# Performance work log

Hardware: AMD Instinct MI355X
Metric: run time of the kernel (lower is better)

Reference implementation:

```python
import jax, jax.numpy as jnp
import numpy as np

B, N = 512, 128
NFEAT, NHID, NHEADS, HID = 133, 60, 8, 300
FP_DIM, FP2, TASK = 1489, 512, 1
ALPHA = 0.2
NEG = -9e15


def _lin(k, fi, fo):
    s = 1.0 / np.sqrt(fi)
    return jax.random.uniform(k, (fi, fo), minval=-s, maxval=s, dtype=jnp.float32)


def _vec(k, fi, n):
    s = 1.0 / np.sqrt(fi)
    return jax.random.uniform(k, (n,), minval=-s, maxval=s, dtype=jnp.float32)


def setup_inputs() -> dict:
    key = jax.random.key(0)
    ks = jax.random.split(key, 24)
    x = jax.random.normal(ks[0], (B, N, NFEAT), dtype=jnp.float32)
    adj = jax.random.randint(ks[1], (B, N, N), 0, 2, dtype=jnp.int32)
    adj = jnp.maximum(adj, jnp.eye(N, dtype=jnp.int32)[None])  # ensure valid softmax rows
    fp = jax.random.uniform(ks[2], (B, FP_DIM), dtype=jnp.float32)
    # multi-head GAT params (W has no bias; attention vector a split into src/dst halves)
    sW = 1.0 / np.sqrt(NFEAT)
    W_heads = jax.random.uniform(ks[3], (NHEADS, NFEAT, NHID), minval=-sW, maxval=sW, dtype=jnp.float32)
    sa = 1.0 / np.sqrt(2 * NHID)
    a_src = jax.random.uniform(ks[4], (NHEADS, NHID), minval=-sa, maxval=sa, dtype=jnp.float32)
    a_dst = jax.random.uniform(ks[5], (NHEADS, NHID), minval=-sa, maxval=sa, dtype=jnp.float32)
    W_out = _lin(ks[6], NHEADS * NHID, HID)
    ao_src = _vec(ks[7], 2 * HID, HID)
    ao_dst = _vec(ks[8], 2 * HID, HID)
    fc1_w = _lin(ks[9], FP_DIM, FP2); fc1_b = _vec(ks[10], FP_DIM, FP2)
    fc2_w = _lin(ks[11], FP2, HID); fc2_b = _vec(ks[12], FP2, HID)
    fcg_w = _lin(ks[13], HID, HID); fcg_b = _vec(ks[14], HID, HID)
    fcf_w = _lin(ks[15], HID, HID); fcf_b = _vec(ks[16], HID, HID)
    ffn1_w = _lin(ks[17], 2 * HID, HID); ffn1_b = _vec(ks[18], 2 * HID, HID)
    ffn2_w = _lin(ks[19], HID, TASK); ffn2_b = _vec(ks[20], HID, TASK)
    return {"x": x, "adj": adj, "fp": fp, "W_heads": W_heads, "a_src": a_src,
            "a_dst": a_dst, "W_out": W_out, "ao_src": ao_src, "ao_dst": ao_dst,
            "fc1_w": fc1_w, "fc1_b": fc1_b, "fc2_w": fc2_w, "fc2_b": fc2_b,
            "fcg_w": fcg_w, "fcg_b": fcg_b, "fcf_w": fcf_w, "fcf_b": fcf_b,
            "ffn1_w": ffn1_w, "ffn1_b": ffn1_b, "ffn2_w": ffn2_w, "ffn2_b": ffn2_b}


def reference(x, adj, fp, W_heads, a_src, a_dst, W_out, ao_src, ao_dst,
              fc1_w, fc1_b, fc2_w, fc2_b, fcg_w, fcg_b, fcf_w, fcf_b,
              ffn1_w, ffn1_b, ffn2_w, ffn2_b):
    adjm = adj > 0  # [B,N,N]
    # --- multi-head GAT layer (dropout = identity in eval) ---
    Wh = jnp.einsum('bnf,hfo->bhno', x, W_heads)              # [B,H,N,nhid]
    s = jnp.einsum('bhno,ho->bhn', Wh, a_src)
    d = jnp.einsum('bhno,ho->bhn', Wh, a_dst)
    # e_ij = leakyrelu(a . [Wh_i ; Wh_j]) without materializing [N,N,2F]
    e = jax.nn.leaky_relu(s[:, :, :, None] + d[:, :, None, :], ALPHA)
    e = jnp.where(adjm[:, None], e, NEG)
    att = jax.nn.softmax(e, axis=-1)                          # softmax over neighbors j
    hp = jax.nn.elu(jnp.einsum('bhnm,bhmo->bhno', att, Wh))   # concat=True head output
    h = hp.transpose(0, 2, 1, 3).reshape(B, N, NHEADS * NHID)
    # --- output GAT layer (concat=False) ---
    Wo = h @ W_out                                            # [B,N,HID]
    eo = jax.nn.leaky_relu((Wo @ ao_src)[:, :, None] + (Wo @ ao_dst)[:, None, :], ALPHA)
    eo = jnp.where(adjm, eo, NEG)
    ho = jax.nn.softmax(eo, axis=-1) @ Wo
    ho = jax.nn.log_softmax(jax.nn.elu(ho), axis=-1)          # log_softmax over features (dim=1 in torch)
    gat = ho.mean(axis=1)                                     # sum over atoms / atom_size
    # --- FPN branch ---
    f = jax.nn.relu(fp @ fc1_w + fc1_b)
    f = f @ fc2_w + fc2_b
    # --- fusion (gat_scale = 0.5) ---
    g = jax.nn.relu(gat @ fcg_w + fcg_b)
    f = jax.nn.relu(f @ fcf_w + fcf_b)
    z = jnp.concatenate([g, f], axis=1)                       # [B, 2*HID]
    z = jax.nn.relu(z @ ffn1_w + ffn1_b)
    z = z @ ffn2_w + ffn2_b
    return jax.nn.sigmoid(z)                                  # is_classif, eval mode
```

## Files before the change

kernel.cpp:

```cpp
#include <hip/hip_runtime.h>
#include <hip/hip_bf16.h>
#include <math.h>
#include <stdint.h>

#define LRA 0.2f

typedef __attribute__((ext_vector_type(8))) short bf16x8;
typedef __attribute__((ext_vector_type(8))) unsigned short u16x8;
typedef __attribute__((ext_vector_type(4))) float f32x4;
typedef unsigned long long u64;

__device__ __forceinline__ unsigned short f2bf(float v) {
  union { __hip_bfloat16 b; unsigned short u; } c;
  c.b = __float2bfloat16(v);
  return c.u;
}
__device__ __forceinline__ float bf2f(unsigned short h) {
  union { float f; unsigned int u; } a; a.u = ((unsigned int)h) << 16;
  return a.f;
}
__device__ __forceinline__ float warp_sum(float v){
  #pragma unroll
  for (int s = 32; s; s >>= 1) v += __shfl_xor(v, s);
  return v;
}

__global__ __launch_bounds__(256) void k_mask(const int* __restrict__ adj, u64* __restrict__ mg){
  const int t = threadIdx.x, lane = t & 63, w = t >> 6, b = blockIdx.x;
  const int* adjb = adj + (size_t)b * 128 * 128;
  for (int i = w * 32; i < w * 32 + 32; ++i) {
    u64 b0 = __ballot(adjb[i * 128 + lane] > 0);
    u64 b1 = __ballot(adjb[i * 128 + 64 + lane] > 0);
    if (lane == 0) { mg[((size_t)b * 128 + i) * 2] = b0; mg[((size_t)b * 128 + i) * 2 + 1] = b1; }
  }
}

__global__ __launch_bounds__(64) void k_prep1(
    const float* __restrict__ Whw, unsigned short* __restrict__ BH, unsigned short* __restrict__ BL)
{
  const int kt = blockIdx.x, nt = blockIdx.y, l = threadIdx.x;
  const int n = nt * 16 + (l & 15), k0 = kt * 32 + (l >> 4) * 8;
  const int hd = n / 60, j = n - hd * 60;
  uint4 hv, lv;
  unsigned int* hp = (unsigned int*)&hv;
  unsigned int* lp = (unsigned int*)&lv;
  #pragma unroll
  for (int p = 0; p < 4; ++p) {
    unsigned short hh[2], ll[2];
    #pragma unroll
    for (int e = 0; e < 2; ++e) {
      const int k = k0 + p * 2 + e;
      const float v = (n < 480 && k < 133) ? Whw[((size_t)hd * 133 + k) * 60 + j] : 0.f;
      const unsigned short h = f2bf(v);
      hh[e] = h; ll[e] = f2bf(v - bf2f(h));
    }
    hp[p] = hh[0] | ((unsigned int)hh[1] << 16);
    lp[p] = ll[0] | ((unsigned int)ll[1] << 16);
  }
  const size_t off = (((size_t)(kt * 32 + nt)) * 64 + l) * 8;
  *(uint4*)&BH[off] = hv;
  *(uint4*)&BL[off] = lv;
}

__global__ __launch_bounds__(64) void k_prep2(
    const float* __restrict__ W, unsigned short* __restrict__ BH, unsigned short* __restrict__ BL)
{
  const int kt = blockIdx.x, nt = blockIdx.y, l = threadIdx.x;
  const int n = nt * 16 + (l & 15), k0 = kt * 32 + (l >> 4) * 8;
  uint4 hv, lv;
  unsigned int* hp = (unsigned int*)&hv;
  unsigned int* lp = (unsigned int*)&lv;
  #pragma unroll
  for (int p = 0; p < 4; ++p) {
    unsigned short hh[2], ll[2];
    #pragma unroll
    for (int e = 0; e < 2; ++e) {
      const int k = k0 + p * 2 + e;
      const float v = (n < 300 && k < 480) ? W[(size_t)k * 300 + n] : 0.f;
      const unsigned short h = f2bf(v);
      hh[e] = h; ll[e] = f2bf(v - bf2f(h));
    }
    hp[p] = hh[0] | ((unsigned int)hh[1] << 16);
    lp[p] = ll[0] | ((unsigned int)ll[1] << 16);
  }
  const size_t off = (((size_t)(kt * 20 + nt)) * 64 + l) * 8;
  *(uint4*)&BH[off] = hv;
  *(uint4*)&BL[off] = lv;
}

__global__ __launch_bounds__(512) void k_gemm1(
    const float* __restrict__ x,
    const unsigned short* __restrict__ BH, const unsigned short* __restrict__ BL,
    unsigned int* __restrict__ buf1)
{
  __shared__ unsigned int Apk[32][32];
  const int t = threadIdx.x, lane = t & 63, w = t >> 6, r = lane & 15, g = lane >> 4;
  const int b = blockIdx.x >> 2, p = blockIdx.x & 3;
  const int row0 = p * 32;
  const float* xb = x + (size_t)b * 128 * 133;
  unsigned int* slab = buf1 + (size_t)b * 61440;

  f32x4 acc[2][4];
  #pragma unroll
  for (int mt = 0; mt < 2; ++mt)
    #pragma unroll
    for (int ntl = 0; ntl < 4; ++ntl) acc[mt][ntl] = (f32x4){0.f,0.f,0.f,0.f};

  for (int kt = 0; kt < 5; ++kt) {
    if (t < 256) {
      const int row_l = t >> 3, sl = t & 7;
      const int k0 = kt * 32 + sl * 4;
      uint4 pk;
      unsigned int* pp = (unsigned int*)&pk;
      #pragma unroll
      for (int e = 0; e < 4; ++e) {
        const int k = k0 + e;
        const float v = (k < 133) ? xb[(size_t)(row0 + row_l) * 133 + k] : 0.f;
        const unsigned short h = f2bf(v);
        pp[e] = ((unsigned int)h << 16) | f2bf(v - bf2f(h));
      }
      *(uint4*)&Apk[row_l][((sl ^ (row_l & 7)) << 2)] = pk;
    }
    bf16x8 bh[4], bl[4];
    #pragma unroll
    for (int ntl = 0; ntl < 4; ++ntl) {
      const int nt = w * 4 + ntl;
      const size_t off = (((size_t)(kt * 32 + nt)) * 64 + lane) * 8;
      bh[ntl] = *(const bf16x8*)&BH[off];
      bl[ntl] = *(const bf16x8*)&BL[off];
    }
    __syncthreads();
    #pragma unroll
    for (int mt = 0; mt < 2; ++mt) {
      const int row_l = mt * 16 + r, key = r & 7;
      const uint4 p0 = *(const uint4*)&Apk[row_l][(((2*g)   ^ key) << 2)];
      const uint4 p1 = *(const uint4*)&Apk[row_l][(((2*g+1) ^ key) << 2)];
      const unsigned int pw[8] = {p0.x,p0.y,p0.z,p0.w,p1.x,p1.y,p1.z,p1.w};
      bf16x8 ah, al;
      #pragma unroll
      for (int e = 0; e < 8; ++e) { ah[e] = (short)(pw[e] >> 16); al[e] = (short)(pw[e] & 0xffffu); }
      #pragma unroll
      for (int ntl = 0; ntl < 4; ++ntl) {
        acc[mt][ntl] = __builtin_amdgcn_mfma_f32_16x16x32_bf16(ah, bh[ntl], acc[mt][ntl], 0,0,0);
        acc[mt][ntl] = __builtin_amdgcn_mfma_f32_16x16x32_bf16(al, bh[ntl], acc[mt][ntl], 0,0,0);
        acc[mt][ntl] = __builtin_amdgcn_mfma_f32_16x16x32_bf16(ah, bl[ntl], acc[mt][ntl], 0,0,0);
      }
    }
    __syncthreads();
  }
  #pragma unroll
  for (int mt = 0; mt < 2; ++mt)
    #pragma unroll
    for (int ntl = 0; ntl < 4; ++ntl) {
      const int cc = (w * 4 + ntl) * 16 + r;
      if (cc < 480) {
        const int hd = cc / 60, cl = cc - hd * 60;
        uint4 pv;
        unsigned int* pp = (unsigned int*)&pv;
        #pragma unroll
        for (int q = 0; q < 4; ++q) {
          const float v = acc[mt][ntl][q];
          const unsigned short h = f2bf(v);
          pp[q] = ((unsigned int)h << 16) | f2bf(v - bf2f(h));
        }
        *(uint4*)&slab[(size_t)hd * 7680 + (size_t)cl * 128 + row0 + mt * 16 + (g << 2)] = pv;
      }
    }
}

__global__ __launch_bounds__(64) void k_sd1(
    const unsigned int* __restrict__ buf1, const float* __restrict__ asrc,
    const float* __restrict__ adst, float* __restrict__ s1g, float* __restrict__ d1g)
{
  const int lane = threadIdx.x, sl = blockIdx.x, hd = sl & 7;
  const unsigned int* slab = buf1 + (size_t)sl * 7680;
  float s0 = 0.f, s1v = 0.f, d0 = 0.f, d1v = 0.f;
  #pragma unroll 4
  for (int c = 0; c < 60; ++c) {
    const float ac = asrc[hd * 60 + c], dc = adst[hd * 60 + c];
    const unsigned int p0 = slab[c * 128 + lane];
    const unsigned int p1 = slab[c * 128 + 64 + lane];
    const float v0 = bf2f((unsigned short)(p0 >> 16)) + bf2f((unsigned short)(p0 & 0xffffu));
    const float v1 = bf2f((unsigned short)(p1 >> 16)) + bf2f((unsigned short)(p1 & 0xffffu));
    s0 += v0 * ac; d0 += v0 * dc;
    s1v += v1 * ac; d1v += v1 * dc;
  }
  s1g[(size_t)sl * 128 + lane] = s0;      d1g[(size_t)sl * 128 + lane] = d0;
  s1g[(size_t)sl * 128 + 64 + lane] = s1v; d1g[(size_t)sl * 128 + 64 + lane] = d1v;
}

__global__ __launch_bounds__(128) void k_sd2(
    const unsigned int* __restrict__ buf1, const float* __restrict__ aos,
    const float* __restrict__ aod, float* __restrict__ s2g, float* __restrict__ d2g)
{
  const int j = threadIdx.x, b = blockIdx.x;
  const unsigned int* slab = buf1 + (size_t)b * 61440;
  float s = 0.f, d = 0.f;
  #pragma unroll 4
  for (int c = 0; c < 300; ++c) {
    const float ac = aos[c], dc = aod[c];
    const unsigned int pk = slab[(size_t)c * 128 + j];
    const float v = bf2f((unsigned short)(pk >> 16)) + bf2f((unsigned short)(pk & 0xffffu));
    s += v * ac; d += v * dc;
  }
  s2g[(size_t)b * 128 + j] = s;
  d2g[(size_t)b * 128 + j] = d;
}

__device__ __forceinline__ float make_att_frags(
    const float si, const u64 ma, const u64 mb2, const float* darr,
    const int g, bf16x8* pah, bf16x8* pal)
{
  const unsigned int mby[4] = {
    (unsigned int)(ma  >> (g * 8)) & 0xffu,
    (unsigned int)(ma  >> (32 + g * 8)) & 0xffu,
    (unsigned int)(mb2 >> (g * 8)) & 0xffu,
    (unsigned int)(mb2 >> (32 + g * 8)) & 0xffu };
  float ev[4][8];
  float mx = -3e38f;
  #pragma unroll
  for (int kt = 0; kt < 4; ++kt)
    #pragma unroll
    for (int e = 0; e < 8; ++e) {
      const int j = ((kt & 1) * 32) + ((kt >> 1) * 64) + g * 8 + e;
      float v = si + darr[j];
      v = fmaxf(v, LRA * v);
      const float vv = (mby[((kt & 1) << 1) | (kt >> 1)] & (1u << e)) ? v : -3e38f;
      ev[kt][e] = vv;
      mx = fmaxf(mx, vv);
    }
  mx = fmaxf(mx, __shfl_xor(mx, 16));
  mx = fmaxf(mx, __shfl_xor(mx, 32));
  float sum = 0.f;
  #pragma unroll
  for (int kt = 0; kt < 4; ++kt)
    #pragma unroll
    for (int e = 0; e < 8; ++e) {
      const float p = (ev[kt][e] > -1e37f) ? __expf(ev[kt][e] - mx) : 0.f;
      ev[kt][e] = p;
      sum += p;
    }
  sum += __shfl_xor(sum, 16);
  sum += __shfl_xor(sum, 32);
  #pragma unroll
  for (int kt = 0; kt < 4; ++kt) {
    const int ks = ((kt & 1) << 1) | (kt >> 1);
    union { unsigned int u[4]; bf16x8 v; } hw, lw;
    #pragma unroll
    for (int p2 = 0; p2 < 4; ++p2) {
      const float p0 = ev[ks][2 * p2], p1 = ev[ks][2 * p2 + 1];
      const unsigned short h0 = f2bf(p0), h1 = f2bf(p1);
      hw.u[p2] = h0 | ((unsigned int)h1 << 16);
      lw.u[p2] = f2bf(p0 - bf2f(h0)) | ((unsigned int)f2bf(p1 - bf2f(h1)) << 16);
    }
    pah[kt] = hw.v;
    pal[kt] = lw.v;
  }
  return 1.f / sum;
}

__global__ __launch_bounds__(256) void k_att1(
    unsigned int* __restrict__ buf1, const u64* __restrict__ mg,
    const float* __restrict__ s1g, const float* __restrict__ d1g)
{
  __shared__ unsigned short Th[16][64][8], Tl[16][64][8];
  __shared__ float sarr[128], darr[128];
  __shared__ u64 mAr[128], mBr[128];
  const int t = threadIdx.x, lane = t & 63, w = t >> 6, r = lane & 15, g = lane >> 4;
  const int bid = blockIdx.x;
  const int lb = ((bid & 7) << 9) | (bid >> 3);
  const int b = lb >> 3, hd = lb & 7;
  const size_t sl = (size_t)b * 8 + hd;
  unsigned int* slab = buf1 + sl * 7680;

  if (t < 128) {
    sarr[t] = s1g[sl * 128 + t];
    darr[t] = d1g[sl * 128 + t];
    mAr[t] = mg[((size_t)b * 128 + t) * 2];
    mBr[t] = mg[((size_t)b * 128 + t) * 2 + 1];
  }
  #pragma unroll
  for (int ii = 0; ii < 4; ++ii) {
    const int idx = t + ii * 256;
    const int c = idx & 63, jg = idx >> 6;
    uint4 p0 = {0,0,0,0}, p1 = {0,0,0,0};
    if (c < 60) {
      const uint4* src = (const uint4*)&slab[(size_t)c * 128 + jg * 8];
      p0 = src[0]; p1 = src[1];
    }
    const unsigned int pw[8] = {p0.x,p0.y,p0.z,p0.w,p1.x,p1.y,p1.z,p1.w};
    u16x8 hv, lv;
    #pragma unroll
    for (int e = 0; e < 8; ++e) { hv[e] = (unsigned short)(pw[e] >> 16); lv[e] = (unsigned short)(pw[e] & 0xffffu); }
    const int tile = ((c >> 4) << 2) | (jg >> 2);
    const int li = ((jg & 3) << 4) | (c & 15);
    *(u16x8*)&Th[tile][li][0] = hv;
    *(u16x8*)&Tl[tile][li][0] = lv;
  }
  __syncthreads();
  bf16x8 pah[2][4], pal[2][4];
  float inv2[2];
  #pragma unroll
  for (int mt = 0; mt < 2; ++mt) {
    const int i = w * 32 + mt * 16 + r;
    inv2[mt] = make_att_frags(sarr[i], mAr[i], mBr[i], darr, g, pah[mt], pal[mt]);
  }
  f32x4 acc[2][4];
  #pragma unroll
  for (int mt = 0; mt < 2; ++mt)
    #pragma unroll
    for (int nt = 0; nt < 4; ++nt) acc[mt][nt] = (f32x4){0.f,0.f,0.f,0.f};
  #pragma unroll
  for (int kt = 0; kt < 4; ++kt)
    #pragma unroll
    for (int nt = 0; nt < 4; ++nt) {
      const bf16x8 bh = *(const bf16x8*)&Th[(nt << 2) | kt][lane][0];
      const bf16x8 bl = *(const bf16x8*)&Tl[(nt << 2) | kt][lane][0];
      #pragma unroll
      for (int mt = 0; mt < 2; ++mt) {
        acc[mt][nt] = __builtin_amdgcn_mfma_f32_16x16x32_bf16(pah[mt][kt], bh, acc[mt][nt], 0,0,0);
        acc[mt][nt] = __builtin_amdgcn_mfma_f32_16x16x32_bf16(pal[mt][kt], bh, acc[mt][nt], 0,0,0);
        acc[mt][nt] = __builtin_amdgcn_mfma_f32_16x16x32_bf16(pah[mt][kt], bl, acc[mt][nt], 0,0,0);
      }
    }
  #pragma unroll
  for (int mt = 0; mt < 2; ++mt) {
    float sc[4];
    #pragma unroll
    for (int q = 0; q < 4; ++q) sc[q] = __shfl(inv2[mt], g * 4 + q);
    #pragma unroll
    for (int nt = 0; nt < 4; ++nt) {
      const int cc = nt * 16 + r;
      if (cc < 60) {
        #pragma unroll
        for (int q = 0; q < 4; ++q) {
          const int row = w * 32 + mt * 16 + g * 4 + q;
          float v = acc[mt][nt][q] * sc[q];
          v = v > 0.f ? v : __expf(v) - 1.f;
          const unsigned short h = f2bf(v), l = f2bf(v - bf2f(h));
          slab[(size_t)row * 60 + cc] = ((unsigned int)h << 16) | l;
        }
      }
    }
  }
}

__global__ __launch_bounds__(256, 3) void k_gemm2(
    unsigned int* __restrict__ buf1,
    const unsigned short* __restrict__ BH, const unsigned short* __restrict__ BL)
{
  __shared__ unsigned int Apk[64][32];
  const int t = threadIdx.x, lane = t & 63, w = t >> 6, r = lane & 15, g = lane >> 4;
  const int b = blockIdx.x >> 1, p = blockIdx.x & 1;
  const int row0 = p * 64;
  unsigned int* slab = buf1 + (size_t)b * 61440;

  f32x4 acc[4][5];
  #pragma unroll
  for (int mt = 0; mt < 4; ++mt)
    #pragma unroll
    for (int ntl = 0; ntl < 5; ++ntl) acc[mt][ntl] = (f32x4){0.f,0.f,0.f,0.f};

  for (int kt = 0; kt < 15; ++kt) {
    #pragma unroll
    for (int i = 0; i < 2; ++i) {
      const int idx = t + i * 256, row_l = idx >> 3, sl = idx & 7;
      const int k0 = kt * 32 + sl * 4;
      const int hd = k0 / 60, c = k0 - hd * 60;
      const uint4 v = *(const uint4*)&slab[(size_t)hd * 7680 + (size_t)(row0 + row_l) * 60 + c];
      *(uint4*)&Apk[row_l][((sl ^ (row_l & 7)) << 2)] = v;
    }
    bf16x8 bh[5], bl[5];
    #pragma unroll
    for (int ntl = 0; ntl < 5; ++ntl) {
      const int nt = w * 5 + ntl;
      const size_t off = (((size_t)(kt * 20 + nt)) * 64 + lane) * 8;
      bh[ntl] = *(const bf16x8*)&BH[off];
      bl[ntl] = *(const bf16x8*)&BL[off];
    }
    __syncthreads();
    #pragma unroll
    for (int mt = 0; mt < 4; ++mt) {
      const int row_l = mt * 16 + r, key = r & 7;
      const uint4 p0 = *(const uint4*)&Apk[row_l][(((2*g)   ^ key) << 2)];
      const uint4 p1 = *(const uint4*)&Apk[row_l][(((2*g+1) ^ key) << 2)];
      const unsigned int pw[8] = {p0.x,p0.y,p0.z,p0.w,p1.x,p1.y,p1.z,p1.w};
      bf16x8 ah, al;
      #pragma unroll
      for (int e = 0; e < 8; ++e) { ah[e] = (short)(pw[e] >> 16); al[e] = (short)(pw[e] & 0xffffu); }
      #pragma unroll
      for (int ntl = 0; ntl < 5; ++ntl) {
        acc[mt][ntl] = __builtin_amdgcn_mfma_f32_16x16x32_bf16(ah, bh[ntl], acc[mt][ntl], 0,0,0);
        acc[mt][ntl] = __builtin_amdgcn_mfma_f32_16x16x32_bf16(al, bh[ntl], acc[mt][ntl], 0,0,0);
        acc[mt][ntl] = __builtin_amdgcn_mfma_f32_16x16x32_bf16(ah, bl[ntl], acc[mt][ntl], 0,0,0);
      }
    }
    __syncthreads();
  }
  #pragma unroll
  for (int mt = 0; mt < 4; ++mt)
    #pragma unroll
    for (int ntl = 0; ntl < 5; ++ntl) {
      const int cc = w * 80 + ntl * 16 + r;
      if (cc < 300) {
        uint4 pv;
        unsigned int* pp = (unsigned int*)&pv;
        #pragma unroll
        for (int q = 0; q < 4; ++q) {
          const float v = acc[mt][ntl][q];
          const unsigned short h = f2bf(v);
          pp[q] = ((unsigned int)h << 16) | f2bf(v - bf2f(h));
        }
        *(uint4*)&slab[(size_t)cc * 128 + row0 + mt * 16 + (g << 2)] = pv;
      }
    }
}

__global__ __launch_bounds__(256) void k_att2(
    const unsigned int* __restrict__ buf1, const u64* __restrict__ mg,
    const float* __restrict__ s2g, const float* __restrict__ d2g,
    float* __restrict__ gat)
{
  __shared__ unsigned short Th[16][64][8], Tl[16][64][8];
  __shared__ float sarr[128], darr[128];
  __shared__ u64 mAr[128], mBr[128];
  __shared__ float colsum[304];
  __shared__ float srow[16];
  const int t = threadIdx.x, lane = t & 63, w = t >> 6, r = lane & 15, g = lane >> 4;
  const int b = blockIdx.x;
  const unsigned int* slab = buf1 + (size_t)b * 61440;

  if (t < 128) {
    sarr[t] = s2g[(size_t)b * 128 + t];
    darr[t] = d2g[(size_t)b * 128 + t];
    mAr[t] = mg[((size_t)b * 128 + t) * 2];
    mBr[t] = mg[((size_t)b * 128 + t) * 2 + 1];
  }
  for (int c = t; c < 304; c += 256) colsum[c] = 0.f;
  __syncthreads();
  bf16x8 pah[2][4], pal[2][4];
  float inv2[2];
  #pragma unroll
  for (int mt = 0; mt < 2; ++mt) {
    const int i = w * 32 + mt * 16 + r;
    inv2[mt] = make_att_frags(sarr[i], mAr[i], mBr[i], darr, g, pah[mt], pal[mt]);
  }
  float scq[2][4];
  #pragma unroll
  for (int mt = 0; mt < 2; ++mt)
    #pragma unroll
    for (int q = 0; q < 4; ++q) scq[mt][q] = __shfl(inv2[mt], g * 4 + q);

  float m8[2][4], l8[2][4];
  #pragma unroll
  for (int mt = 0; mt < 2; ++mt)
    #pragma unroll
    for (int q = 0; q < 4; ++q) { m8[mt][q] = -3e38f; l8[mt][q] = 0.f; }

  for (int ch = 0; ch < 5; ++ch) {
    #pragma unroll
    for (int ii = 0; ii < 4; ++ii) {
      const int idx = t + ii * 256;
      const int c = idx & 63, jg = idx >> 6;
      const int gc = ch * 64 + c;
      uint4 p0 = {0,0,0,0}, p1 = {0,0,0,0};
      if (gc < 300) {
        const uint4* src = (const uint4*)&slab[(size_t)gc * 128 + jg * 8];
        p0 = src[0]; p1 = src[1];
      }
      const unsigned int pw[8] = {p0.x,p0.y,p0.z,p0.w,p1.x,p1.y,p1.z,p1.w};
      u16x8 hv, lv;
      #pragma unroll
      for (int e = 0; e < 8; ++e) { hv[e] = (unsigned short)(pw[e] >> 16); lv[e] = (unsigned short)(pw[e] & 0xffffu); }
      const int tile = ((c >> 4) << 2) | (jg >> 2);
      const int li = ((jg & 3) << 4) | (c & 15);
      *(u16x8*)&Th[tile][li][0] = hv;
      *(u16x8*)&Tl[tile][li][0] = lv;
    }
    __syncthreads();
    f32x4 pacc[2][4];
    #pragma unroll
    for (int mt = 0; mt < 2; ++mt)
      #pragma unroll
      for (int nt = 0; nt < 4; ++nt) pacc[mt][nt] = (f32x4){0.f,0.f,0.f,0.f};
    #pragma unroll
    for (int kt = 0; kt < 4; ++kt)
      #pragma unroll
      for (int nt = 0; nt < 4; ++nt) {
        const bf16x8 bh = *(const bf16x8*)&Th[(nt << 2) | kt][lane][0];
        const bf16x8 bl = *(const bf16x8*)&Tl[(nt << 2) | kt][lane][0];
        #pragma unroll
        for (int mt = 0; mt < 2; ++mt) {
          pacc[mt][nt] = __builtin_amdgcn_mfma_f32_16x16x32_bf16(pah[mt][kt], bh, pacc[mt][nt], 0,0,0);
          pacc[mt][nt] = __builtin_amdgcn_mfma_f32_16x16x32_bf16(pal[mt][kt], bh, pacc[mt][nt], 0,0,0);
          pacc[mt][nt] = __builtin_amdgcn_mfma_f32_16x16x32_bf16(pah[mt][kt], bl, pacc[mt][nt], 0,0,0);
        }
      }
    float csA[4] = {0,0,0,0};
    #pragma unroll
    for (int mt = 0; mt < 2; ++mt) {
      float vq[4][4];
      #pragma unroll
      for (int nt = 0; nt < 4; ++nt) {
        const int cc = ch * 64 + nt * 16 + r;
        const bool cv = cc < 300;
        #pragma unroll
        for (int q = 0; q < 4; ++q) {
          float v = pacc[mt][nt][q] * scq[mt][q];
          v = v > 0.f ? v : __expf(v) - 1.f;
          vq[nt][q] = cv ? v : -3e38f;
          csA[nt] += cv ? v : 0.f;
        }
      }
      #pragma unroll
      for (int q = 0; q < 4; ++q) {
        float mx = fmaxf(fmaxf(vq[0][q], vq[1][q]), fmaxf(vq[2][q], vq[3][q]));
        mx = fmaxf(mx, __shfl_xor(mx, 1));
        mx = fmaxf(mx, __shfl_xor(mx, 2));
        mx = fmaxf(mx, __shfl_xor(mx, 4));
        mx = fmaxf(mx, __shfl_xor(mx, 8));
        const float nm = fmaxf(m8[mt][q], mx);
        float ps = __expf(vq[0][q]-nm) + __expf(vq[1][q]-nm) + __expf(vq[2][q]-nm) + __expf(vq[3][q]-nm);
        ps += __shfl_xor(ps, 1); ps += __shfl_xor(ps, 2);
        ps += __shfl_xor(ps, 4); ps += __shfl_xor(ps, 8);
        l8[mt][q] = l8[mt][q] * __expf(m8[mt][q] - nm) + ps;
        m8[mt][q] = nm;
      }
    }
    #pragma unroll
    for (int nt = 0; nt < 4; ++nt) {
      float cs = csA[nt];
      cs += __shfl_xor(cs, 16); cs += __shfl_xor(cs, 32);
      const int cc = ch * 64 + nt * 16 + r;
      if (g == 0 && cc < 300) atomicAdd(&colsum[cc], cs);
    }
    __syncthreads();
  }
  if (r == 0) {
    float sp = 0.f;
    #pragma unroll
    for (int mt = 0; mt < 2; ++mt)
      #pragma unroll
      for (int q = 0; q < 4; ++q) sp += m8[mt][q] + __logf(l8[mt][q]);
    srow[w * 4 + g] = sp;
  }
  __syncthreads();
  float S = 0.f;
  #pragma unroll
  for (int k = 0; k < 16; ++k) S += srow[k];
  for (int c = t; c < 300; c += 256)
    gat[(size_t)b * 300 + c] = (colsum[c] - S) * (1.f / 128.f);
}

__global__ __launch_bounds__(256) void k_gemm_sk(
    const float* __restrict__ A, const float* __restrict__ B,
    float* __restrict__ P, int M, int K, int N, int kpt)
{
  __shared__ unsigned short Ah[64][40], Al[64][40], Bh[64][40], Bl[64][40];
  const int t = threadIdx.x, lane = t & 63, w = t >> 6, r = lane & 15, g = lane >> 4;
  const int row0 = blockIdx.x * 64, col0 = blockIdx.y * 64;
  const int sk = blockIdx.z;
  const int k0 = sk * kpt * 32;
  const int kend = min(K, k0 + kpt * 32);

  f32x4 acc[4];
  #pragma unroll
  for (int nt = 0; nt < 4; ++nt) acc[nt] = (f32x4){0.f,0.f,0.f,0.f};

  for (int kt = k0; kt < kend; kt += 32) {
    #pragma unroll
    for (int ii = 0; ii < 2; ++ii) {
      const int idx = t + ii * 256, ar = idx >> 3, aq = (idx & 7) * 4, gk = kt + aq;
      const float* ap = &A[(size_t)(row0 + ar) * K + gk];
      float v0 = gk     < kend ? ap[0] : 0.f;
      float v1 = gk + 1 < kend ? ap[1] : 0.f;
      float v2 = gk + 2 < kend ? ap[2] : 0.f;
      float v3 = gk + 3 < kend ? ap[3] : 0.f;
      unsigned short h0=f2bf(v0),h1=f2bf(v1),h2=f2bf(v2),h3=f2bf(v3);
      *(unsigned int*)&Ah[ar][aq]   = h0 | ((unsigned int)h1 << 16);
      *(unsigned int*)&Ah[ar][aq+2] = h2 | ((unsigned int)h3 << 16);
      unsigned short l0=f2bf(v0-bf2f(h0)),l1=f2bf(v1-bf2f(h1)),l2=f2bf(v2-bf2f(h2)),l3=f2bf(v3-bf2f(h3));
      *(unsigned int*)&Al[ar][aq]   = l0 | ((unsigned int)l1 << 16);
      *(unsigned int*)&Al[ar][aq+2] = l2 | ((unsigned int)l3 << 16);
    }
    #pragma unroll
    for (int ii = 0; ii < 4; ++ii) {
      const int idx = t + ii * 256, n = idx & 63, kk = (idx >> 6) * 2;
      const int gn = col0 + n;
      float v0 = (gn < N && kt + kk     < kend) ? B[(size_t)(kt + kk) * N + gn] : 0.f;
      float v1 = (gn < N && kt + kk + 1 < kend) ? B[(size_t)(kt + kk + 1) * N + gn] : 0.f;
      unsigned short h0 = f2bf(v0), h1 = f2bf(v1);
      *(unsigned int*)&Bh[n][kk] = h0 | ((unsigned int)h1 << 16);
      unsigned short l0 = f2bf(v0 - bf2f(h0)), l1 = f2bf(v1 - bf2f(h1));
      *(unsigned int*)&Bl[n][kk] = l0 | ((unsigned int)l1 << 16);
    }
    __syncthreads();
    const bf16x8 ah  = *(const bf16x8*)&Ah[w * 16 + r][g * 8];
    const bf16x8 al2 = *(const bf16x8*)&Al[w * 16 + r][g * 8];
    #pragma unroll
    for (int nt = 0; nt < 4; ++nt) {
      const bf16x8 bh = *(const bf16x8*)&Bh[nt * 16 + r][g * 8];
      const bf16x8 bl = *(const bf16x8*)&Bl[nt * 16 + r][g * 8];
      acc[nt] = __builtin_amdgcn_mfma_f32_16x16x32_bf16(ah,  bh, acc[nt], 0,0,0);
      acc[nt] = __builtin_amdgcn_mfma_f32_16x16x32_bf16(al2, bh, acc[nt], 0,0,0);
      acc[nt] = __builtin_amdgcn_mfma_f32_16x16x32_bf16(ah,  bl, acc[nt], 0,0,0);
    }
    __syncthreads();
  }
  float* Pout = P + (size_t)sk * M * N;
  #pragma unroll
  for (int nt = 0; nt < 4; ++nt) {
    const int cc = col0 + nt * 16 + r;
    if (cc < N) {
      #pragma unroll
      for (int q = 0; q < 4; ++q)
        Pout[(size_t)(row0 + w * 16 + g * 4 + q) * N + cc] = acc[nt][q];
    }
  }
}

__global__ __launch_bounds__(256) void k_reduce(
    const float* __restrict__ P, const float* __restrict__ bias,
    float* __restrict__ C, int M, int N, int ldc, int nsk, int act)
{
  const int idx = blockIdx.x * 256 + threadIdx.x;
  if (idx >= M * N) return;
  const int row = idx / N, col = idx - row * N;
  float s = bias[col];
  for (int k = 0; k < nsk; ++k) s += P[(size_t)k * M * N + idx];
  if (act) s = fmaxf(s, 0.f);
  C[(size_t)row * ldc + col] = s;
}

__global__ __launch_bounds__(512) void k_out(
    const float* __restrict__ z1, const float* __restrict__ w2,
    const float* __restrict__ b2, float* __restrict__ out)
{
  const int t = threadIdx.x, lane = t & 63, w = t >> 6;
  const int b = blockIdx.x * 8 + w;
  float p = 0.f;
  for (int k = lane; k < 300; k += 64) p += z1[(size_t)b * 300 + k] * w2[k];
  p = warp_sum(p);
  if (lane == 0) out[b] = 1.f / (1.f + __expf(-(p + b2[0])));
}

extern "C" void kernel_launch(void* const* d_in, const int* in_sizes, int n_in,
                              void* d_out, int out_size, void* d_ws, size_t ws_size,
                              hipStream_t stream)
{
  const float* x    = (const float*)d_in[0];
  const int*   adj  = (const int*)d_in[1];
  const float* fp   = (const float*)d_in[2];
  const float* Whw  = (const float*)d_in[3];
  const float* asrc = (const float*)d_in[4];
  const float* adst = (const float*)d_in[5];
  const float* Wout = (const float*)d_in[6];
  const float* aos  = (const float*)d_in[7];
  const float* aod  = (const float*)d_in[8];
  const float* fc1w = (const float*)d_in[9];
  const float* fc1b = (const float*)d_in[10];
  const float* fc2w = (const float*)d_in[11];
  const float* fc2b = (const float*)d_in[12];
  const float* fcgw = (const float*)d_in[13];
  const float* fcgb = (const float*)d_in[14];
  const float* fcfw = (const float*)d_in[15];
  const float* fcfb = (const float*)d_in[16];
  const float* f1w  = (const float*)d_in[17];
  const float* f1b  = (const float*)d_in[18];
  const float* f2w  = (const float*)d_in[19];
  const float* f2b  = (const float*)d_in[20];
  float* out = (float*)d_out;

  char* wsb = (char*)d_ws;
  unsigned int* buf1 = (unsigned int*)wsb;
  float* s1g = (float*)(wsb + 125829120);
  float* d1g = (float*)(wsb + 127926272);
  float* s2g = (float*)(wsb + 130023424);
  float* d2g = (float*)(wsb + 130285568);
  u64*   mgb = (u64*)  (wsb + 130547712);
  float* gatp = (float*)(wsb + 131596288);
  float* fpnp = (float*)(wsb + 132210688);
  float* f1buf = (float*)(wsb + 132825088);
  float* zb    = (float*)(wsb + 133873664);
  float* z1b   = (float*)(wsb + 135102464);
  float* P0 = (float*)(wsb + 135716864);
  float* P1 = (float*)(wsb + 142008320);
  float* P2 = (float*)(wsb + 144465920);
  float* P3 = (float*)(wsb + 145694720);
  float* P4 = (float*)(wsb + 146923520);
  unsigned short* Bf1H = (unsigned short*)(wsb + 149381120);
  unsigned short* Bf1L = (unsigned short*)(wsb + 149544960);
  unsigned short* Bf2H = (unsigned short*)(wsb + 149708800);
  unsigned short* Bf2L = (unsigned short*)(wsb + 150016000);

  k_prep1<<<dim3(5, 32), 64, 0, stream>>>(Whw, Bf1H, Bf1L);
  k_prep2<<<dim3(15, 20), 64, 0, stream>>>(Wout, Bf2H, Bf2L);
  k_mask <<<512, 256, 0, stream>>>(adj, mgb);
  k_gemm1<<<2048, 512, 0, stream>>>(x, Bf1H, Bf1L, buf1);
  k_sd1  <<<4096, 64, 0, stream>>>(buf1, asrc, adst, s1g, d1g);
  k_att1 <<<4096, 256, 0, stream>>>(buf1, mgb, s1g, d1g);
  k_gemm2<<<1024, 256, 0, stream>>>(buf1, Bf2H, Bf2L);
  k_sd2  <<<512, 128, 0, stream>>>(buf1, aos, aod, s2g, d2g);
  k_att2 <<<512, 256, 0, stream>>>(buf1, mgb, s2g, d2g, gatp);
  k_gemm_sk<<<dim3(8,8,6), 256, 0, stream>>>(fp, fc1w, P0, 512, 1489, 512, 8);
  k_reduce<<<1024, 256, 0, stream>>>(P0, fc1b, f1buf, 512, 512, 512, 6, 1);
  k_gemm_sk<<<dim3(8,5,4), 256, 0, stream>>>(f1buf, fc2w, P1, 512, 512, 300, 4);
  k_reduce<<<600, 256, 0, stream>>>(P1, fc2b, fpnp, 512, 300, 300, 4, 0);
  k_gemm_sk<<<dim3(8,5,2), 256, 0, stream>>>(gatp, fcgw, P2, 512, 300, 300, 5);
  k_gemm_sk<<<dim3(8,5,2), 256, 0, stream>>>(fpnp, fcfw, P3, 512, 300, 300, 5);
  k_reduce<<<600, 256, 0, stream>>>(P2, fcgb, zb, 512, 300, 600, 2, 1);
  k_reduce<<<600, 256, 0, stream>>>(P3, fcfb, zb + 300, 512, 300, 600, 2, 1);
  k_gemm_sk<<<dim3(8,5,4), 256, 0, stream>>>(zb, f1w, P4, 512, 600, 300, 5);
  k_reduce<<<600, 256, 0, stream>>>(P4, f1b, z1b, 512, 300, 300, 4, 1);
  k_out<<<64, 512, 0, stream>>>(z1b, f2w, f2b, out);
}
```

Before: 383.8 us.

## Fuse first-layer GEMM, attention scores and per-head attention into one kernel

Replaces the separate k_gemm1, k_sd1 and k_att1 kernels with a single k_fga1 kernel. Each block computes one head's Wh for one graph in registers, derives the src/dst scores from the accumulators with shuffles, and stages the split-bf16 Wh in LDS for the attention MFMA. The intermediate global round-trip of Wh and the score buffers is removed. In exchange, x is reloaded and reconverted eight times (once per head), and the LDS footprint per block is larger.

After: 385.9 us. No clear change (+0.5%).

```diff
diff --git a/kernel.cpp b/kernel.cpp
--- a/kernel.cpp
+++ b/kernel.cpp
@@ -40,7 +40,7 @@
 {
   const int kt = blockIdx.x, nt = blockIdx.y, l = threadIdx.x;
   const int n = nt * 16 + (l & 15), k0 = kt * 32 + (l >> 4) * 8;
-  const int hd = n / 60, j = n - hd * 60;
+  const int hd = n >> 6, j = n & 63;
   uint4 hv, lv;
   unsigned int* hp = (unsigned int*)&hv;
   unsigned int* lp = (unsigned int*)&lv;
@@ -50,7 +50,7 @@
     #pragma unroll
     for (int e = 0; e < 2; ++e) {
       const int k = k0 + p * 2 + e;
-      const float v = (n < 480 && k < 133) ? Whw[((size_t)hd * 133 + k) * 60 + j] : 0.f;
+      const float v = (j < 60 && k < 133) ? Whw[((size_t)hd * 133 + k) * 60 + j] : 0.f;
       const unsigned short h = f2bf(v);
       hh[e] = h; ll[e] = f2bf(v - bf2f(h));
     }
@@ -86,125 +86,6 @@
   const size_t off = (((size_t)(kt * 20 + nt)) * 64 + l) * 8;
   *(uint4*)&BH[off] = hv;
   *(uint4*)&BL[off] = lv;
-}
-
-__global__ __launch_bounds__(512) void k_gemm1(
-    const float* __restrict__ x,
-    const unsigned short* __restrict__ BH, const unsigned short* __restrict__ BL,
-    unsigned int* __restrict__ buf1)
-{
-  __shared__ unsigned int Apk[32][32];
-  const int t = threadIdx.x, lane = t & 63, w = t >> 6, r = lane & 15, g = lane >> 4;
-  const int b = blockIdx.x >> 2, p = blockIdx.x & 3;
-  const int row0 = p * 32;
-  const float* xb = x + (size_t)b * 128 * 133;
-  unsigned int* slab = buf1 + (size_t)b * 61440;
-
-  f32x4 acc[2][4];
-  #pragma unroll
-  for (int mt = 0; mt < 2; ++mt)
-    #pragma unroll
-    for (int ntl = 0; ntl < 4; ++ntl) acc[mt][ntl] = (f32x4){0.f,0.f,0.f,0.f};
-
-  for (int kt = 0; kt < 5; ++kt) {
-    if (t < 256) {
-      const int row_l = t >> 3, sl = t & 7;
-      const int k0 = kt * 32 + sl * 4;
-      uint4 pk;
-      unsigned int* pp = (unsigned int*)&pk;
-      #pragma unroll
-      for (int e = 0; e < 4; ++e) {
-        const int k = k0 + e;
-        const float v = (k < 133) ? xb[(size_t)(row0 + row_l) * 133 + k] : 0.f;
-        const unsigned short h = f2bf(v);
-        pp[e] = ((unsigned int)h << 16) | f2bf(v - bf2f(h));
-      }
-      *(uint4*)&Apk[row_l][((sl ^ (row_l & 7)) << 2)] = pk;
-    }
-    bf16x8 bh[4], bl[4];
-    #pragma unroll
-    for (int ntl = 0; ntl < 4; ++ntl) {
-      const int nt = w * 4 + ntl;
-      const size_t off = (((size_t)(kt * 32 + nt)) * 64 + lane) * 8;
-      bh[ntl] = *(const bf16x8*)&BH[off];
-      bl[ntl] = *(const bf16x8*)&BL[off];
-    }
-    __syncthreads();
-    #pragma unroll
-    for (int mt = 0; mt < 2; ++mt) {
-      const int row_l = mt * 16 + r, key = r & 7;
-      const uint4 p0 = *(const uint4*)&Apk[row_l][(((2*g)   ^ key) << 2)];
-      const uint4 p1 = *(const uint4*)&Apk[row_l][(((2*g+1) ^ key) << 2)];
-      const unsigned int pw[8] = {p0.x,p0.y,p0.z,p0.w,p1.x,p1.y,p1.z,p1.w};
-      bf16x8 ah, al;
-      #pragma unroll
-      for (int e = 0; e < 8; ++e) { ah[e] = (short)(pw[e] >> 16); al[e] = (short)(pw[e] & 0xffffu); }
-      #pragma unroll
-      for (int ntl = 0; ntl < 4; ++ntl) {
-        acc[mt][ntl] = __builtin_amdgcn_mfma_f32_16x16x32_bf16(ah, bh[ntl], acc[mt][ntl], 0,0,0);
-        acc[mt][ntl] = __builtin_amdgcn_mfma_f32_16x16x32_bf16(al, bh[ntl], acc[mt][ntl], 0,0,0);
-        acc[mt][ntl] = __builtin_amdgcn_mfma_f32_16x16x32_bf16(ah, bl[ntl], acc[mt][ntl], 0,0,0);
-      }
-    }
-    __syncthreads();
-  }
-  #pragma unroll
-  for (int mt = 0; mt < 2; ++mt)
-    #pragma unroll
-    for (int ntl = 0; ntl < 4; ++ntl) {
-      const int cc = (w * 4 + ntl) * 16 + r;
-      if (cc < 480) {
-        const int hd = cc / 60, cl = cc - hd * 60;
-        uint4 pv;
-        unsigned int* pp = (unsigned int*)&pv;
-        #pragma unroll
-        for (int q = 0; q < 4; ++q) {
-          const float v = acc[mt][ntl][q];
-          const unsigned short h = f2bf(v);
-          pp[q] = ((unsigned int)h << 16) | f2bf(v - bf2f(h));
-        }
-        *(uint4*)&slab[(size_t)hd * 7680 + (size_t)cl * 128 + row0 + mt * 16 + (g << 2)] = pv;
-      }
-    }
-}
-
-__global__ __launch_bounds__(64) void k_sd1(
-    const unsigned int* __restrict__ buf1, const float* __restrict__ asrc,
-    const float* __restrict__ adst, float* __restrict__ s1g, float* __restrict__ d1g)
-{
-  const int lane = threadIdx.x, sl = blockIdx.x, hd = sl & 7;
-  const unsigned int* slab = buf1 + (size_t)sl * 7680;
-  float s0 = 0.f, s1v = 0.f, d0 = 0.f, d1v = 0.f;
-  #pragma unroll 4
-  for (int c = 0; c < 60; ++c) {
-    const float ac = asrc[hd * 60 + c], dc = adst[hd * 60 + c];
-    const unsigned int p0 = slab[c * 128 + lane];
-    const unsigned int p1 = slab[c * 128 + 64 + lane];
-    const float v0 = bf2f((unsigned short)(p0 >> 16)) + bf2f((unsigned short)(p0 & 0xffffu));
-    const float v1 = bf2f((unsigned short)(p1 >> 16)) + bf2f((unsigned short)(p1 & 0xffffu));
-    s0 += v0 * ac; d0 += v0 * dc;
-    s1v += v1 * ac; d1v += v1 * dc;
-  }
-  s1g[(size_t)sl * 128 + lane] = s0;      d1g[(size_t)sl * 128 + lane] = d0;
-  s1g[(size_t)sl * 128 + 64 + lane] = s1v; d1g[(size_t)sl * 128 + 64 + lane] = d1v;
-}
-
-__global__ __launch_bounds__(128) void k_sd2(
-    const unsigned int* __restrict__ buf1, const float* __restrict__ aos,
-    const float* __restrict__ aod, float* __restrict__ s2g, float* __restrict__ d2g)
-{
-  const int j = threadIdx.x, b = blockIdx.x;
-  const unsigned int* slab = buf1 + (size_t)b * 61440;
-  float s = 0.f, d = 0.f;
-  #pragma unroll 4
-  for (int c = 0; c < 300; ++c) {
-    const float ac = aos[c], dc = aod[c];
-    const unsigned int pk = slab[(size_t)c * 128 + j];
-    const float v = bf2f((unsigned short)(pk >> 16)) + bf2f((unsigned short)(pk & 0xffffu));
-    s += v * ac; d += v * dc;
-  }
-  s2g[(size_t)b * 128 + j] = s;
-  d2g[(size_t)b * 128 + j] = d;
 }
 
 __device__ __forceinline__ float make_att_frags(
@@ -259,86 +140,151 @@
   return 1.f / sum;
 }
 
-__global__ __launch_bounds__(256) void k_att1(
-    unsigned int* __restrict__ buf1, const u64* __restrict__ mg,
-    const float* __restrict__ s1g, const float* __restrict__ d1g)
-{
-  __shared__ unsigned short Th[16][64][8], Tl[16][64][8];
+__global__ __launch_bounds__(512) void k_fga1(
+    const float* __restrict__ x,
+    const unsigned short* __restrict__ BH, const unsigned short* __restrict__ BL,
+    const float* __restrict__ asrc, const float* __restrict__ adst,
+    const u64* __restrict__ mg, unsigned int* __restrict__ buf1)
+{
+  __shared__ unsigned int Apk[128][32];
+  __shared__ unsigned int Whp[64][132];
+  __shared__ float asl[64], adl[64];
   __shared__ float sarr[128], darr[128];
   __shared__ u64 mAr[128], mBr[128];
   const int t = threadIdx.x, lane = t & 63, w = t >> 6, r = lane & 15, g = lane >> 4;
-  const int bid = blockIdx.x;
-  const int lb = ((bid & 7) << 9) | (bid >> 3);
-  const int b = lb >> 3, hd = lb & 7;
-  const size_t sl = (size_t)b * 8 + hd;
-  unsigned int* slab = buf1 + sl * 7680;
-
+  const int hd = blockIdx.x >> 9, b = blockIdx.x & 511;
+  const float* xb = x + (size_t)b * 128 * 133;
+  unsigned int* slab = buf1 + (size_t)b * 61440;
+
+  if (t < 64) {
+    asl[t] = (t < 60) ? asrc[hd * 60 + t] : 0.f;
+    adl[t] = (t < 60) ? adst[hd * 60 + t] : 0.f;
+  }
   if (t < 128) {
-    sarr[t] = s1g[sl * 128 + t];
-    darr[t] = d1g[sl * 128 + t];
     mAr[t] = mg[((size_t)b * 128 + t) * 2];
     mBr[t] = mg[((size_t)b * 128 + t) * 2 + 1];
   }
-  #pragma unroll
-  for (int ii = 0; ii < 4; ++ii) {
-    const int idx = t + ii * 256;
-    const int c = idx & 63, jg = idx >> 6;
-    uint4 p0 = {0,0,0,0}, p1 = {0,0,0,0};
-    if (c < 60) {
-      const uint4* src = (const uint4*)&slab[(size_t)c * 128 + jg * 8];
-      p0 = src[0]; p1 = src[1];
-    }
-    const unsigned int pw[8] = {p0.x,p0.y,p0.z,p0.w,p1.x,p1.y,p1.z,p1.w};
-    u16x8 hv, lv;
-    #pragma unroll
-    for (int e = 0; e < 8; ++e) { hv[e] = (unsigned short)(pw[e] >> 16); lv[e] = (unsigned short)(pw[e] & 0xffffu); }
-    const int tile = ((c >> 4) << 2) | (jg >> 2);
-    const int li = ((jg & 3) << 4) | (c & 15);
-    *(u16x8*)&Th[tile][li][0] = hv;
-    *(u16x8*)&Tl[tile][li][0] = lv;
+
+  f32x4 acc[4];
+  #pragma unroll
+  for (int ntl = 0; ntl < 4; ++ntl) acc[ntl] = (f32x4){0.f,0.f,0.f,0.f};
+
+  for (int kt = 0; kt < 5; ++kt) {
+    #pragma unroll
+    for (int i = 0; i < 2; ++i) {
+      const int idx = t + i * 512, row_l = idx >> 3, sl = idx & 7;
+      const int k0 = kt * 32 + sl * 4;
+      uint4 pk;
+      unsigned int* pp = (unsigned int*)&pk;
+      #pragma unroll
+      for (int e = 0; e < 4; ++e) {
+        const int k = k0 + e;
+        const float v = (k < 133) ? xb[(size_t)row_l * 133 + k] : 0.f;
+        const unsigned short h = f2bf(v);
+        pp[e] = ((unsigned int)h << 16) | f2bf(v - bf2f(h));
+      }
+      *(uint4*)&Apk[row_l][((sl ^ (row_l & 7)) << 2)] = pk;
+    }
+    bf16x8 bh[4], bl[4];
+    #pragma unroll
+    for (int ntl = 0; ntl < 4; ++ntl) {
+      const size_t off = (((size_t)(kt * 32 + hd * 4 + ntl)) * 64 + lane) * 8;
+      bh[ntl] = *(const bf16x8*)&BH[off];
+      bl[ntl] = *(const bf16x8*)&BL[off];
+    }
+    __syncthreads();
+    {
+      const int row_l = w * 16 + r, key = r & 7;
+      const uint4 p0 = *(const uint4*)&Apk[row_l][(((2*g)   ^ key) << 2)];
+      const uint4 p1 = *(const uint4*)&Apk[row_l][(((2*g+1) ^ key) << 2)];
+      const unsigned int pw[8] = {p0.x,p0.y,p0.z,p0.w,p1.x,p1.y,p1.z,p1.w};
+      bf16x8 ah, al;
+      #pragma unroll
+      for (int e = 0; e < 8; ++e) { ah[e] = (short)(pw[e] >> 16); al[e] = (short)(pw[e] & 0xffffu); }
+      #pragma unroll
+      for (int ntl = 0; ntl < 4; ++ntl) {
+        acc[ntl] = __builtin_amdgcn_mfma_f32_16x16x32_bf16(ah, bh[ntl], acc[ntl], 0,0,0);
+        acc[ntl] = __builtin_amdgcn_mfma_f32_16x16x32_bf16(al, bh[ntl], acc[ntl], 0,0,0);
+        acc[ntl] = __builtin_amdgcn_mfma_f32_16x16x32_bf16(ah, bl[ntl], acc[ntl], 0,0,0);
+      }
+    }
+    __syncthreads();
+  }
+
+  {
+    float sv[4] = {0,0,0,0}, dv[4] = {0,0,0,0};
+    #pragma unroll
+    for (int ntl = 0; ntl < 4; ++ntl) {
+      const int cl = ntl * 16 + r;
+      const float as = asl[cl], ad = adl[cl];
+      #pragma unroll
+      for (int q = 0; q < 4; ++q) { sv[q] += acc[ntl][q] * as; dv[q] += acc[ntl][q] * ad; }
+    }
+    #pragma unroll
+    for (int q = 0; q < 4; ++q) {
+      #pragma unroll
+      for (int s = 1; s <= 8; s <<= 1) { sv[q] += __shfl_xor(sv[q], s); dv[q] += __shfl_xor(dv[q], s); }
+    }
+    if (r == 0) {
+      #pragma unroll
+      for (int q = 0; q < 4; ++q) {
+        sarr[w * 16 + g * 4 + q] = sv[q];
+        darr[w * 16 + g * 4 + q] = dv[q];
+      }
+    }
+  }
+  #pragma unroll
+  for (int ntl = 0; ntl < 4; ++ntl) {
+    const int c = ntl * 16 + r;
+    uint4 pv;
+    unsigned int* pp = (unsigned int*)&pv;
+    #pragma unroll
+    for (int q = 0; q < 4; ++q) {
+      const float v = acc[ntl][q];
+      const unsigned short h = f2bf(v);
+      pp[q] = ((unsigned int)h << 16) | f2bf(v - bf2f(h));
+    }
+    *(uint4*)&Whp[c][w * 16 + (g << 2)] = pv;
   }
   __syncthreads();
-  bf16x8 pah[2][4], pal[2][4];
-  float inv2[2];
-  #pragma unroll
-  for (int mt = 0; mt < 2; ++mt) {
-    const int i = w * 32 + mt * 16 + r;
-    inv2[mt] = make_att_frags(sarr[i], mAr[i], mBr[i], darr, g, pah[mt], pal[mt]);
-  }
-  f32x4 acc[2][4];
-  #pragma unroll
-  for (int mt = 0; mt < 2; ++mt)
-    #pragma unroll
-    for (int nt = 0; nt < 4; ++nt) acc[mt][nt] = (f32x4){0.f,0.f,0.f,0.f};
-  #pragma unroll
-  for (int kt = 0; kt < 4; ++kt)
-    #pragma unroll
-    for (int nt = 0; nt < 4; ++nt) {
-      const bf16x8 bh = *(const bf16x8*)&Th[(nt << 2) | kt][lane][0];
-      const bf16x8 bl = *(const bf16x8*)&Tl[(nt << 2) | kt][lane][0];
-      #pragma unroll
-      for (int mt = 0; mt < 2; ++mt) {
-        acc[mt][nt] = __builtin_amdgcn_mfma_f32_16x16x32_bf16(pah[mt][kt], bh, acc[mt][nt], 0,0,0);
-        acc[mt][nt] = __builtin_amdgcn_mfma_f32_16x16x32_bf16(pal[mt][kt], bh, acc[mt][nt], 0,0,0);
-        acc[mt][nt] = __builtin_amdgcn_mfma_f32_16x16x32_bf16(pah[mt][kt], bl, acc[mt][nt], 0,0,0);
-      }
-    }
-  #pragma unroll
-  for (int mt = 0; mt < 2; ++mt) {
+
+  bf16x8 pah[4], pal[4];
+  const float inv = make_att_frags(sarr[w * 16 + r], mAr[w * 16 + r], mBr[w * 16 + r],
+                                   darr, g, pah, pal);
+  f32x4 pacc[4];
+  #pragma unroll
+  for (int ntl = 0; ntl < 4; ++ntl) pacc[ntl] = (f32x4){0.f,0.f,0.f,0.f};
+  #pragma unroll
+  for (int kt = 0; kt < 4; ++kt) {
+    #pragma unroll
+    for (int ntl = 0; ntl < 4; ++ntl) {
+      const int c = ntl * 16 + r;
+      const uint4 q0 = *(const uint4*)&Whp[c][kt * 32 + g * 8];
+      const uint4 q1 = *(const uint4*)&Whp[c][kt * 32 + g * 8 + 4];
+      const unsigned int pw[8] = {q0.x,q0.y,q0.z,q0.w,q1.x,q1.y,q1.z,q1.w};
+      bf16x8 bh, bl;
+      #pragma unroll
+      for (int e = 0; e < 8; ++e) { bh[e] = (short)(pw[e] >> 16); bl[e] = (short)(pw[e] & 0xffffu); }
+      pacc[ntl] = __builtin_amdgcn_mfma_f32_16x16x32_bf16(pah[kt], bh, pacc[ntl], 0,0,0);
+      pacc[ntl] = __builtin_amdgcn_mfma_f32_16x16x32_bf16(pal[kt], bh, pacc[ntl], 0,0,0);
+      pacc[ntl] = __builtin_amdgcn_mfma_f32_16x16x32_bf16(pah[kt], bl, pacc[ntl], 0,0,0);
+    }
+  }
+  {
     float sc[4];
     #pragma unroll
-    for (int q = 0; q < 4; ++q) sc[q] = __shfl(inv2[mt], g * 4 + q);
-    #pragma unroll
-    for (int nt = 0; nt < 4; ++nt) {
-      const int cc = nt * 16 + r;
+    for (int q = 0; q < 4; ++q) sc[q] = __shfl(inv, g * 4 + q);
+    #pragma unroll
+    for (int ntl = 0; ntl < 4; ++ntl) {
+      const int cc = ntl * 16 + r;
       if (cc < 60) {
         #pragma unroll
         for (int q = 0; q < 4; ++q) {
-          const int row = w * 32 + mt * 16 + g * 4 + q;
-          float v = acc[mt][nt][q] * sc[q];
+          const int row = w * 16 + g * 4 + q;
+          float v = pacc[ntl][q] * sc[q];
           v = v > 0.f ? v : __expf(v) - 1.f;
           const unsigned short h = f2bf(v), l = f2bf(v - bf2f(h));
-          slab[(size_t)row * 60 + cc] = ((unsigned int)h << 16) | l;
+          slab[(size_t)hd * 7680 + (size_t)row * 60 + cc] = ((unsigned int)h << 16) | l;
         }
       }
     }
@@ -414,6 +360,24 @@
         *(uint4*)&slab[(size_t)cc * 128 + row0 + mt * 16 + (g << 2)] = pv;
       }
     }
+}
+
+__global__ __launch_bounds__(128) void k_sd2(
+    const unsigned int* __restrict__ buf1, const float* __restrict__ aos,
+    const float* __restrict__ aod, float* __restrict__ s2g, float* __restrict__ d2g)
+{
+  const int j = threadIdx.x, b = blockIdx.x;
+  const unsigned int* slab = buf1 + (size_t)b * 61440;
+  float s = 0.f, d = 0.f;
+  #pragma unroll 4
+  for (int c = 0; c < 300; ++c) {
+    const float ac = aos[c], dc = aod[c];
+    const unsigned int pk = slab[(size_t)c * 128 + j];
+    const float v = bf2f((unsigned short)(pk >> 16)) + bf2f((unsigned short)(pk & 0xffffu));
+    s += v * ac; d += v * dc;
+  }
+  s2g[(size_t)b * 128 + j] = s;
+  d2g[(size_t)b * 128 + j] = d;
 }
 
 __global__ __launch_bounds__(256) void k_att2(
@@ -673,8 +637,6 @@
 
   char* wsb = (char*)d_ws;
   unsigned int* buf1 = (unsigned int*)wsb;
-  float* s1g = (float*)(wsb + 125829120);
-  float* d1g = (float*)(wsb + 127926272);
   float* s2g = (float*)(wsb + 130023424);
   float* d2g = (float*)(wsb + 130285568);
   u64*   mgb = (u64*)  (wsb + 130547712);
@@ -696,9 +658,7 @@
   k_prep1<<<dim3(5, 32), 64, 0, stream>>>(Whw, Bf1H, Bf1L);
   k_prep2<<<dim3(15, 20), 64, 0, stream>>>(Wout, Bf2H, Bf2L);
   k_mask <<<512, 256, 0, stream>>>(adj, mgb);
-  k_gemm1<<<2048, 512, 0, stream>>>(x, Bf1H, Bf1L, buf1);
-  k_sd1  <<<4096, 64, 0, stream>>>(buf1, asrc, adst, s1g, d1g);
-  k_att1 <<<4096, 256, 0, stream>>>(buf1, mgb, s1g, d1g);
+  k_fga1 <<<4096, 512, 0, stream>>>(x, Bf1H, Bf1L, asrc, adst, mgb, buf1);
   k_gemm2<<<1024, 256, 0, stream>>>(buf1, Bf2H, Bf2L);
   k_sd2  <<<512, 128, 0, stream>>>(buf1, aos, aod, s2g, d2g);
   k_att2 <<<512, 256, 0, stream>>>(buf1, mgb, s2g, d2g, gatp);
```
